# Kernel tuning notes

Hardware: AMD Instinct MI355X
Metric: run time of the kernel (lower is better)

## Reference

```python
import jax, jax.numpy as jnp
import numpy as np

EPS = 1e-5  # clamp floor in BitNet activation quantization


def _bitnet_act_quant(x):
    # Match transformers.integrations.bitnet.ActQuant: per-last-dim int8 fake-quant.
    scale = 127.0 / jnp.clip(jnp.max(jnp.abs(x), axis=-1, keepdims=True), EPS)
    return jnp.clip(jnp.round(x * scale), -128.0, 127.0) / scale


def setup_inputs() -> dict:
    key = jax.random.key(0)
    k1, k2, k3, k4 = jax.random.split(key, 4)
    B, S, D, O = 1, 4096, 4096, 4096  # batch, seq_len, in_features, out_features
    x = jax.random.normal(k1, (B, S, D), dtype=jnp.float32)
    # Ternary weight matrix in {-1, 0, +1} (what the bit-packed RSR format encodes).
    W = jax.random.randint(k2, (O, D), -1, 2).astype(jnp.float32)
    bias = jax.random.normal(k3, (O,), dtype=jnp.float32) * 0.01
    # BitNet weight_scale (divide mode): positive scalar.
    weight_scale = jax.random.uniform(k4, (), dtype=jnp.float32, minval=0.5, maxval=2.0)
    return {"x": x, "W": W, "bias": bias, "weight_scale": weight_scale}


def reference(x, W, bias, weight_scale):
    # CPU backend path: BitNet activation fake-quant, then ternary GEMV per token.
    q = _bitnet_act_quant(x.astype(jnp.float32))
    out = jnp.einsum('bsd,od->bso', q, W)  # [B, S, O]
    out = out + bias
    out = out / weight_scale  # weight_scale_mode == 'divide'
    return out.astype(x.dtype)
```

## Files before the change

kernel.cpp:

```cpp
#include <hip/hip_runtime.h>
#include <hip/hip_bf16.h>


#define SEQ  4096
#define DIM  4096
#define OUTD 4096

typedef int i32x4 __attribute__((ext_vector_type(4)));
typedef unsigned char u8;

__device__ __forceinline__ void gload16(const void* g, void* lds) {
    __builtin_amdgcn_global_load_lds(
        (const __attribute__((address_space(1))) void*)g,
        (__attribute__((address_space(3))) void*)lds, 16, 0, 0);
}

__device__ __forceinline__ int ldsoff(int r, int kq) {
    const int rp = r >> 1;
    const int w = (((r & 1) << 6) | (kq << 4)) ^ ((rp & 3) << 4);
    return rp * 128 + w;
}

__global__ __launch_bounds__(256) void quant_kernel(
    const float* __restrict__ x, char* __restrict__ q, float* __restrict__ rscale) {
    const int row = blockIdx.x;
    const int t = threadIdx.x;
    const int lane = t & 63, wave = t >> 6;
    const float4* xr = (const float4*)(x + (size_t)row * DIM);

    float4 r[4];
    float m = 0.0f;
#pragma unroll
    for (int i = 0; i < 4; ++i) {
        r[i] = xr[t + 256 * i];
        m = fmaxf(m, fmaxf(fmaxf(fabsf(r[i].x), fabsf(r[i].y)),
                           fmaxf(fabsf(r[i].z), fabsf(r[i].w))));
    }
#pragma unroll
    for (int off = 32; off > 0; off >>= 1)
        m = fmaxf(m, __shfl_xor(m, off, 64));
    __shared__ float red[4];
    if (lane == 0) red[wave] = m;
    __syncthreads();
    const float amax = fmaxf(fmaxf(red[0], red[1]), fmaxf(red[2], red[3]));
    const float scale = 127.0f / fmaxf(amax, 1e-5f);
    if (t == 0) rscale[row] = 1.0f / scale;

    char4* qr = (char4*)(q + (size_t)row * DIM);
#pragma unroll
    for (int i = 0; i < 4; ++i) {
        float q0 = fminf(127.0f, fmaxf(-128.0f, rintf(r[i].x * scale)));
        float q1 = fminf(127.0f, fmaxf(-128.0f, rintf(r[i].y * scale)));
        float q2 = fminf(127.0f, fmaxf(-128.0f, rintf(r[i].z * scale)));
        float q3 = fminf(127.0f, fmaxf(-128.0f, rintf(r[i].w * scale)));
        char4 o;
        o.x = (signed char)q0; o.y = (signed char)q1;
        o.z = (signed char)q2; o.w = (signed char)q3;
        qr[t + 256 * i] = o;
    }
}

__global__ __launch_bounds__(256) void wconv_kernel(
    const float4* __restrict__ W4, char4* __restrict__ Wb4, int n4) {
    int i = blockIdx.x * blockDim.x + threadIdx.x;
    const int stride = gridDim.x * blockDim.x;
    for (; i < n4; i += stride) {
        float4 w = W4[i];
        char4 o;
        o.x = (signed char)w.x; o.y = (signed char)w.y;
        o.z = (signed char)w.z; o.w = (signed char)w.w;
        Wb4[i] = o;
    }
}

__global__ __launch_bounds__(512, 2) void gemm_kernel(
    const u8* __restrict__ A, const u8* __restrict__ B,
    const float* __restrict__ rscale, const float* __restrict__ bias,
    const float* __restrict__ wscale, float* __restrict__ out) {
    __shared__ __align__(16) u8 As[4 * 16384];
    __shared__ __align__(16) u8 Bs[4 * 16384];
    const int tid = threadIdx.x;
    const int lane = tid & 63, wave = tid >> 6;
    const int wr = wave >> 2, wc = wave & 3;
    const int fr = lane & 15, kq = lane >> 4;

    const int bid = blockIdx.x;
    const int swz = (bid & 7) * 32 + (bid >> 3);
    const int brow = swz >> 4, bcol = swz & 15;

    const int v = (tid & 7) ^ ((tid >> 3) & 3);
    const int kb = (v & 3) * 16;
    const int r0 = ((tid >> 3) << 1) + (v >> 2);
    const u8* gA0 = A + (size_t)(brow * 256 + r0) * DIM + kb;
    const u8* gA1 = A + (size_t)(brow * 256 + 128 + r0) * DIM + kb;
    const u8* gB0 = B + (size_t)(bcol * 256 + r0) * DIM + kb;
    const u8* gB1 = B + (size_t)(bcol * 256 + 128 + r0) * DIM + kb;
    u8* lA0 = &As[tid * 16];
    u8* lA1 = &As[8192 + tid * 16];
    u8* lB0 = &Bs[tid * 16];
    u8* lB1 = &Bs[8192 + tid * 16];

#define STAGE(T, S) do { const int _k = (T) * 64;          \
        gload16(gA0 + _k, lA0 + (S) * 16384);              \
        gload16(gA1 + _k, lA1 + (S) * 16384);              \
        gload16(gB0 + _k, lB0 + (S) * 16384);              \
        gload16(gB1 + _k, lB1 + (S) * 16384); } while (0)

    int aoff[8], boff[4];
#pragma unroll
    for (int m = 0; m < 8; ++m) aoff[m] = ldsoff(wr * 128 + m * 16 + fr, kq);
#pragma unroll
    for (int n = 0; n < 4; ++n) boff[n] = ldsoff(wc * 64 + n * 16 + fr, kq);

    i32x4 acc[8][4] = {};

#define COMPUTE(S) do {                                                        \
        i32x4 af[8], bfv[4];                                                   \
        _Pragma("unroll")                                                      \
        for (int n = 0; n < 4; ++n)                                            \
            bfv[n] = *(const i32x4*)&Bs[(S) * 16384 + boff[n]];                \
        _Pragma("unroll")                                                      \
        for (int m = 0; m < 8; ++m)                                            \
            af[m] = *(const i32x4*)&As[(S) * 16384 + aoff[m]];                 \
        _Pragma("unroll")                                                      \
        for (int m = 0; m < 8; ++m)                                            \
            _Pragma("unroll")                                                  \
            for (int n = 0; n < 4; ++n)                                        \
                acc[m][n] = __builtin_amdgcn_mfma_i32_16x16x64_i8(             \
                    af[m], bfv[n], acc[m][n], 0, 0, 0);                        \
    } while (0)

#define VMW(N) asm volatile("s_waitcnt vmcnt(" #N ")" ::: "memory")
#define BAR()  do { asm volatile("" ::: "memory");                             \
                    __builtin_amdgcn_s_barrier();                              \
                    asm volatile("" ::: "memory"); } while (0)

    STAGE(0, 0); STAGE(1, 1); STAGE(2, 2);

    for (int tb = 0; tb < 15; ++tb) {
        const int t = tb * 4;
        VMW(8); BAR(); STAGE(t + 3, 3); COMPUTE(0);
        VMW(8); BAR(); STAGE(t + 4, 0); COMPUTE(1);
        VMW(8); BAR(); STAGE(t + 5, 1); COMPUTE(2);
        VMW(8); BAR(); STAGE(t + 6, 2); COMPUTE(3);
    }
    VMW(8); BAR(); STAGE(63, 3); COMPUTE(0);
    VMW(8); BAR(); COMPUTE(1);
    VMW(4); BAR(); COMPUTE(2);
    VMW(0); BAR(); COMPUTE(3);

    const float invws = 1.0f / wscale[0];
    const int rr0 = brow * 256 + wr * 128 + (kq << 2);
    const int c0 = bcol * 256 + wc * 64 + fr;
    float bv[4];
#pragma unroll
    for (int n = 0; n < 4; ++n) bv[n] = bias[c0 + n * 16] * invws;
#pragma unroll
    for (int m = 0; m < 8; ++m) {
#pragma unroll
        for (int j = 0; j < 4; ++j) {
            const int r = rr0 + m * 16 + j;
            const float rs = rscale[r] * invws;
            float* orow = out + (size_t)r * OUTD + c0;
#pragma unroll
            for (int n = 0; n < 4; ++n)
                orow[n * 16] = (float)acc[m][n][j] * rs + bv[n];
        }
    }
#undef STAGE
#undef COMPUTE
#undef VMW
#undef BAR
}

extern "C" void kernel_launch(void* const* d_in, const int* in_sizes, int n_in,
                              void* d_out, int out_size, void* d_ws, size_t ws_size,
                              hipStream_t stream) {
    const float* x      = (const float*)d_in[0];
    const float* W      = (const float*)d_in[1];
    const float* bias   = (const float*)d_in[2];
    const float* wscale = (const float*)d_in[3];
    float* out = (float*)d_out;

    char* ws = (char*)d_ws;
    char* q_i8 = ws;
    char* w_i8 = ws + (size_t)16777216;
    float* rscale = (float*)(ws + (size_t)33554432);

    quant_kernel<<<SEQ, 256, 0, stream>>>(x, q_i8, rscale);
    wconv_kernel<<<4096, 256, 0, stream>>>((const float4*)W, (char4*)w_i8,
                                           (OUTD * DIM) / 4);
    gemm_kernel<<<256, 512, 0, stream>>>((const u8*)q_i8, (const u8*)w_i8,
                                         rscale, bias, wscale, out);
}
```

Measured before the change: 92.88 us.

## Merge quant and weight-convert kernels; switch GEMM to double-buffered 128-K stages

Merges the activation quantization and weight conversion into a single launch, with the first SEQ blocks quantizing rows and the remaining blocks converting weights. The GEMM pipeline changes from a 4-stage ring of 64-wide K tiles to 2 stages of 128-wide K tiles. Each stage now runs two MFMA passes per barrier and reissues its loads only after a second barrier. Larger chunks halve the barrier count per K, but prefetch depth drops and each iteration adds an extra barrier before the loads are issued, so load latency may be less well hidden.

```diff
diff --git a/kernel.cpp b/kernel.cpp
--- a/kernel.cpp
+++ b/kernel.cpp
@@ -21,55 +21,55 @@
     return rp * 128 + w;
 }
 
-__global__ __launch_bounds__(256) void quant_kernel(
-    const float* __restrict__ x, char* __restrict__ q, float* __restrict__ rscale) {
-    const int row = blockIdx.x;
+__global__ __launch_bounds__(256) void prep_kernel(
+    const float* __restrict__ x, char* __restrict__ q, float* __restrict__ rscale,
+    const float4* __restrict__ W4, char4* __restrict__ Wb4) {
+    const int bid = blockIdx.x;
     const int t = threadIdx.x;
-    const int lane = t & 63, wave = t >> 6;
-    const float4* xr = (const float4*)(x + (size_t)row * DIM);
-
-    float4 r[4];
-    float m = 0.0f;
+    if (bid < SEQ) {
+        const int row = bid;
+        const int lane = t & 63, wave = t >> 6;
+        const float4* xr = (const float4*)(x + (size_t)row * DIM);
+        float4 r[4];
+        float m = 0.0f;
 #pragma unroll
-    for (int i = 0; i < 4; ++i) {
-        r[i] = xr[t + 256 * i];
-        m = fmaxf(m, fmaxf(fmaxf(fabsf(r[i].x), fabsf(r[i].y)),
-                           fmaxf(fabsf(r[i].z), fabsf(r[i].w))));
-    }
+        for (int i = 0; i < 4; ++i) {
+            r[i] = xr[t + 256 * i];
+            m = fmaxf(m, fmaxf(fmaxf(fabsf(r[i].x), fabsf(r[i].y)),
+                               fmaxf(fabsf(r[i].z), fabsf(r[i].w))));
+        }
 #pragma unroll
-    for (int off = 32; off > 0; off >>= 1)
-        m = fmaxf(m, __shfl_xor(m, off, 64));
-    __shared__ float red[4];
-    if (lane == 0) red[wave] = m;
-    __syncthreads();
-    const float amax = fmaxf(fmaxf(red[0], red[1]), fmaxf(red[2], red[3]));
-    const float scale = 127.0f / fmaxf(amax, 1e-5f);
-    if (t == 0) rscale[row] = 1.0f / scale;
-
-    char4* qr = (char4*)(q + (size_t)row * DIM);
+        for (int off = 32; off > 0; off >>= 1)
+            m = fmaxf(m, __shfl_xor(m, off, 64));
+        __shared__ float red[4];
+        if (lane == 0) red[wave] = m;
+        __syncthreads();
+        const float amax = fmaxf(fmaxf(red[0], red[1]), fmaxf(red[2], red[3]));
+        const float scale = 127.0f / fmaxf(amax, 1e-5f);
+        if (t == 0) rscale[row] = 1.0f / scale;
+        char4* qr = (char4*)(q + (size_t)row * DIM);
 #pragma unroll
-    for (int i = 0; i < 4; ++i) {
-        float q0 = fminf(127.0f, fmaxf(-128.0f, rintf(r[i].x * scale)));
-        float q1 = fminf(127.0f, fmaxf(-128.0f, rintf(r[i].y * scale)));
-        float q2 = fminf(127.0f, fmaxf(-128.0f, rintf(r[i].z * scale)));
-        float q3 = fminf(127.0f, fmaxf(-128.0f, rintf(r[i].w * scale)));
-        char4 o;
-        o.x = (signed char)q0; o.y = (signed char)q1;
-        o.z = (signed char)q2; o.w = (signed char)q3;
-        qr[t + 256 * i] = o;
-    }
-}
-
-__global__ __launch_bounds__(256) void wconv_kernel(
-    const float4* __restrict__ W4, char4* __restrict__ Wb4, int n4) {
-    int i = blockIdx.x * blockDim.x + threadIdx.x;
-    const int stride = gridDim.x * blockDim.x;
-    for (; i < n4; i += stride) {
-        float4 w = W4[i];
-        char4 o;
-        o.x = (signed char)w.x; o.y = (signed char)w.y;
-        o.z = (signed char)w.z; o.w = (signed char)w.w;
-        Wb4[i] = o;
+        for (int i = 0; i < 4; ++i) {
+            float q0 = fminf(127.0f, fmaxf(-128.0f, rintf(r[i].x * scale)));
+            float q1 = fminf(127.0f, fmaxf(-128.0f, rintf(r[i].y * scale)));
+            float q2 = fminf(127.0f, fmaxf(-128.0f, rintf(r[i].z * scale)));
+            float q3 = fminf(127.0f, fmaxf(-128.0f, rintf(r[i].w * scale)));
+            char4 o;
+            o.x = (signed char)q0; o.y = (signed char)q1;
+            o.z = (signed char)q2; o.w = (signed char)q3;
+            qr[t + 256 * i] = o;
+        }
+    } else {
+        const int n4 = (OUTD * DIM) / 4;
+        int i = (bid - SEQ) * 256 + t;
+        const int stride = SEQ * 256;
+        for (; i < n4; i += stride) {
+            float4 w = W4[i];
+            char4 o;
+            o.x = (signed char)w.x; o.y = (signed char)w.y;
+            o.z = (signed char)w.z; o.w = (signed char)w.w;
+            Wb4[i] = o;
+        }
     }
 }
 
@@ -77,8 +77,8 @@
     const u8* __restrict__ A, const u8* __restrict__ B,
     const float* __restrict__ rscale, const float* __restrict__ bias,
     const float* __restrict__ wscale, float* __restrict__ out) {
-    __shared__ __align__(16) u8 As[4 * 16384];
-    __shared__ __align__(16) u8 Bs[4 * 16384];
+    __shared__ __align__(16) u8 As[2 * 2 * 16384];
+    __shared__ __align__(16) u8 Bs[2 * 2 * 16384];
     const int tid = threadIdx.x;
     const int lane = tid & 63, wave = tid >> 6;
     const int wr = wave >> 2, wc = wave & 3;
@@ -100,11 +100,16 @@
     u8* lB0 = &Bs[tid * 16];
     u8* lB1 = &Bs[8192 + tid * 16];
 
-#define STAGE(T, S) do { const int _k = (T) * 64;          \
-        gload16(gA0 + _k, lA0 + (S) * 16384);              \
-        gload16(gA1 + _k, lA1 + (S) * 16384);              \
-        gload16(gB0 + _k, lB0 + (S) * 16384);              \
-        gload16(gB1 + _k, lB1 + (S) * 16384); } while (0)
+#define STAGE(T, S) do {                                                       \
+        _Pragma("unroll")                                                      \
+        for (int _u = 0; _u < 2; ++_u) {                                       \
+            const int _k = (T) * 128 + _u * 64;                                \
+            const int _d = (S) * 32768 + _u * 16384;                           \
+            gload16(gA0 + _k, lA0 + _d);                                       \
+            gload16(gA1 + _k, lA1 + _d);                                       \
+            gload16(gB0 + _k, lB0 + _d);                                       \
+            gload16(gB1 + _k, lB1 + _d);                                       \
+        } } while (0)
 
     int aoff[8], boff[4];
 #pragma unroll
@@ -114,14 +119,15 @@
 
     i32x4 acc[8][4] = {};
 
-#define COMPUTE(S) do {                                                        \
+#define COMPUTE(S, U) do {                                                     \
+        const int _b = (S) * 32768 + (U) * 16384;                              \
         i32x4 af[8], bfv[4];                                                   \
         _Pragma("unroll")                                                      \
+        for (int m = 0; m < 8; ++m)                                            \
+            af[m] = *(const i32x4*)&As[_b + aoff[m]];                          \
+        _Pragma("unroll")                                                      \
         for (int n = 0; n < 4; ++n)                                            \
-            bfv[n] = *(const i32x4*)&Bs[(S) * 16384 + boff[n]];                \
-        _Pragma("unroll")                                                      \
-        for (int m = 0; m < 8; ++m)                                            \
-            af[m] = *(const i32x4*)&As[(S) * 16384 + aoff[m]];                 \
+            bfv[n] = *(const i32x4*)&Bs[_b + boff[n]];                         \
         _Pragma("unroll")                                                      \
         for (int m = 0; m < 8; ++m)                                            \
             _Pragma("unroll")                                                  \
@@ -135,19 +141,15 @@
                     __builtin_amdgcn_s_barrier();                              \
                     asm volatile("" ::: "memory"); } while (0)
 
-    STAGE(0, 0); STAGE(1, 1); STAGE(2, 2);
+    STAGE(0, 0); STAGE(1, 1);
 
     for (int tb = 0; tb < 15; ++tb) {
-        const int t = tb * 4;
-        VMW(8); BAR(); STAGE(t + 3, 3); COMPUTE(0);
-        VMW(8); BAR(); STAGE(t + 4, 0); COMPUTE(1);
-        VMW(8); BAR(); STAGE(t + 5, 1); COMPUTE(2);
-        VMW(8); BAR(); STAGE(t + 6, 2); COMPUTE(3);
+        const int t = tb * 2;
+        VMW(8); BAR(); COMPUTE(0, 0); COMPUTE(0, 1); BAR(); STAGE(t + 2, 0);
+        VMW(8); BAR(); COMPUTE(1, 0); COMPUTE(1, 1); BAR(); STAGE(t + 3, 1);
     }
-    VMW(8); BAR(); STAGE(63, 3); COMPUTE(0);
-    VMW(8); BAR(); COMPUTE(1);
-    VMW(4); BAR(); COMPUTE(2);
-    VMW(0); BAR(); COMPUTE(3);
+    VMW(8); BAR(); COMPUTE(0, 0); COMPUTE(0, 1);
+    VMW(0); BAR(); COMPUTE(1, 0); COMPUTE(1, 1);
 
     const float invws = 1.0f / wscale[0];
     const int rr0 = brow * 256 + wr * 128 + (kq << 2);
@@ -187,9 +189,8 @@
     char* w_i8 = ws + (size_t)16777216;
     float* rscale = (float*)(ws + (size_t)33554432);
 
-    quant_kernel<<<SEQ, 256, 0, stream>>>(x, q_i8, rscale);
-    wconv_kernel<<<4096, 256, 0, stream>>>((const float4*)W, (char4*)w_i8,
-                                           (OUTD * DIM) / 4);
+    prep_kernel<<<SEQ + 4096, 256, 0, stream>>>(
+        x, q_i8, rscale, (const float4*)W, (char4*)w_i8);
     gemm_kernel<<<256, 512, 0, stream>>>((const u8*)q_i8, (const u8*)w_i8,
                                          rscale, bias, wscale, out);
 }
```

After: 95.43 us. 1.03x slower.
